# Kernel tuning notes

Measured on AMD Instinct MI355X. Metric: run time of the kernel, lower is better.

Reference implementation:

```python
import jax, jax.numpy as jnp
import numpy as np

D_MODEL = 1024
N_HEADS = 16
D_K = D_MODEL // N_HEADS


def setup_inputs() -> dict:
    key = jax.random.key(0)
    ks = jax.random.split(key, 10)
    B, L = 2, 2048
    s = 1.0 / np.sqrt(D_MODEL)
    inp = {
        "x": jax.random.normal(ks[0], (B, L, D_MODEL), dtype=jnp.float32),
        "bond_influence": jax.random.uniform(ks[1], (B, L, L), dtype=jnp.float32),
        "Wq": jax.random.uniform(ks[2], (D_MODEL, D_MODEL), jnp.float32, -s, s),
        "bq": jax.random.uniform(ks[3], (D_MODEL,), jnp.float32, -s, s),
        "Wk": jax.random.uniform(ks[4], (D_MODEL, D_MODEL), jnp.float32, -s, s),
        "bk": jax.random.uniform(ks[5], (D_MODEL,), jnp.float32, -s, s),
        "Wv": jax.random.uniform(ks[6], (D_MODEL, D_MODEL), jnp.float32, -s, s),
        "bv": jax.random.uniform(ks[7], (D_MODEL,), jnp.float32, -s, s),
        "Wo": jax.random.uniform(ks[8], (D_MODEL, D_MODEL), jnp.float32, -s, s),
        "bo": jax.random.uniform(ks[9], (D_MODEL,), jnp.float32, -s, s),
    }
    return inp


def reference(x, bond_influence, Wq, bq, Wk, bk, Wv, bv, Wo, bo):
    B, L, _ = x.shape
    # QKV projections -> [B, H, L, d_k]
    def proj(W, b):
        return (x @ W + b).reshape(B, L, N_HEADS, D_K).transpose(0, 2, 1, 3)
    Q = proj(Wq, bq)
    K = proj(Wk, bk)
    V = proj(Wv, bv)
    # scores: [B, H, L, L], scaled then modulated by per-batch bond influence
    scores = jnp.einsum('bhqd,bhkd->bhqk', Q, K) / jnp.sqrt(jnp.float32(D_K))
    scores = scores * bond_influence[:, None, :, :]
    attn = jax.nn.softmax(scores, axis=-1)
    out = jnp.einsum('bhqk,bhkd->bhqd', attn, V)  # [B, H, L, d_k]
    out = out.transpose(0, 2, 1, 3).reshape(B, L, D_MODEL)
    return out @ Wo + bo
```

## Files before the change

### kernel.cpp

```cpp
#include <hip/hip_runtime.h>
#include <stdint.h>

typedef unsigned short u16;
typedef __attribute__((ext_vector_type(8))) short bf16x8;
typedef __attribute__((ext_vector_type(4))) float f32x4;

__device__ __forceinline__ u16 f2bf(float f) {
    union { float f; uint32_t u; } v; v.f = f;
    uint32_t u = v.u + 0x7fffu + ((v.u >> 16) & 1u);
    return (u16)(u >> 16);
}
__device__ __forceinline__ float vexp2(float x) {
    float d;
    asm("v_exp_f32 %0, %1" : "=v"(d) : "v"(x));
    return d;
}
__device__ __forceinline__ uint32_t cvtpk(float a, float b) {
    uint32_t d;
    asm("v_cvt_pk_bf16_f32 %0, %1, %2" : "=v"(d) : "v"(a), "v"(b));
    return d;
}

__device__ __forceinline__ void gld16(const void* g, void* l) {
    __builtin_amdgcn_global_load_lds((const __attribute__((address_space(1))) void*)g,
                                     (__attribute__((address_space(3))) void*)l,
                                     16, 0, 0);
}

__device__ __forceinline__ void plswap16(uint32_t& a, uint32_t& b) {
    asm volatile("v_permlane16_swap_b32 %0, %1" : "+v"(a), "+v"(b));
}


__global__ void cvt_bf16_kernel(const float* __restrict__ s, u16* __restrict__ d, int n4,
                                float scale) {
    int i = blockIdx.x * blockDim.x + threadIdx.x;
    const int stride = gridDim.x * blockDim.x;
    for (; i < n4; i += stride) {
        float4 v = ((const float4*)s)[i];
        ushort4 o;
        o.x = f2bf(v.x * scale); o.y = f2bf(v.y * scale);
        o.z = f2bf(v.z * scale); o.w = f2bf(v.w * scale);
        ((ushort4*)d)[i] = o;
    }
}

__global__ void transpose4_bf16_kernel(const float* __restrict__ Wq, const float* __restrict__ Wk,
                                       const float* __restrict__ Wv, const float* __restrict__ Wo,
                                       u16* __restrict__ dqkv, u16* __restrict__ dо) {
    __shared__ float tile[32][33];
    const int z = blockIdx.z;
    const float* src = (z == 0) ? Wq : (z == 1) ? Wk : (z == 2) ? Wv : Wo;
    u16* dst = (z < 3) ? (dqkv + (size_t)z * 1024 * 1024) : dо;
    const int tx = threadIdx.x, ty = threadIdx.y;
    const int bx = blockIdx.x * 32, by = blockIdx.y * 32;
#pragma unroll
    for (int i = ty; i < 32; i += 8)
        tile[i][tx] = src[(size_t)(by + i) * 1024 + bx + tx];
    __syncthreads();
#pragma unroll
    for (int i = ty; i < 32; i += 8)
        dst[(size_t)(bx + i) * 1024 + by + tx] = f2bf(tile[tx][i]);
}


template <int EPI>
__global__ __launch_bounds__(256) void gemm128(
    const u16* __restrict__ A, const u16* __restrict__ Bt,
    const float* __restrict__ bias0, const float* __restrict__ bias1,
    const float* __restrict__ bias2,
    u16* __restrict__ o_q, u16* __restrict__ o_k, u16* __restrict__ o_vt,
    float* __restrict__ o_f)
{
    constexpr int K = 1024;
    __shared__ u16 As[128 * 32];
    __shared__ u16 Bs[128 * 32];
    const int t = threadIdx.x;
    const int lane = t & 63, w = t >> 6;
    const int wm = w >> 1, wn = w & 1;
    const int g = lane >> 4, r = lane & 15;
    const int mbase = blockIdx.y * 128, nbase = blockIdx.x * 128;

    const f32x4 zero4 = {0.f, 0.f, 0.f, 0.f};
    f32x4 acc[4][4];
#pragma unroll
    for (int m = 0; m < 4; ++m)
#pragma unroll
        for (int n = 0; n < 4; ++n) acc[m][n] = zero4;

    for (int k0 = 0; k0 < K; k0 += 32) {
#pragma unroll
        for (int i = 0; i < 2; ++i) {
            const int base = i * 256 + (w << 6);
            const int idx = base + lane;
            const int row = idx >> 2, cc = (idx & 3) << 3;
            gld16(A + (size_t)(mbase + row) * K + k0 + cc, (char*)As + base * 16);
            gld16(Bt + (size_t)(nbase + row) * K + k0 + cc, (char*)Bs + base * 16);
        }
        __syncthreads();

        bf16x8 af[4], bfr[4];
#pragma unroll
        for (int m = 0; m < 4; ++m)
            af[m] = *(const bf16x8*)&As[(wm * 64 + m * 16 + r) * 32 + g * 8];
#pragma unroll
        for (int n = 0; n < 4; ++n)
            bfr[n] = *(const bf16x8*)&Bs[(wn * 64 + n * 16 + r) * 32 + g * 8];
        __builtin_amdgcn_s_setprio(1);
#pragma unroll
        for (int m = 0; m < 4; ++m)
#pragma unroll
            for (int n = 0; n < 4; ++n)
                acc[m][n] = __builtin_amdgcn_mfma_f32_16x16x32_bf16(af[m], bfr[n], acc[m][n], 0, 0, 0);
        __builtin_amdgcn_s_setprio(0);
        __syncthreads();
    }

#pragma unroll
    for (int m = 0; m < 4; ++m) {
#pragma unroll
        for (int n = 0; n < 4; ++n) {
            const int c = nbase + wn * 64 + n * 16 + r;
#pragma unroll
            for (int j = 0; j < 4; ++j) {
                const int rr = mbase + wm * 64 + m * 16 + g * 4 + j;
                const float y = acc[m][n][j];
                if (EPI == 0) {
                    const int which = c >> 10, d = c & 1023;
                    const int b = rr >> 11, l = rr & 2047;
                    const int h = d >> 6, dd = d & 63;
                    const size_t bh = (size_t)(b * 16 + h);
                    if (which == 0) {
                        o_q[(bh * 2048 + l) * 64 + dd] = f2bf((y + bias0[d]) * 0.18033688011112042f);
                    } else if (which == 1) {
                        o_k[(bh * 2048 + l) * 64 + dd] = f2bf(y + bias1[d]);
                    } else {
                        o_vt[(bh * 64 + dd) * 2048 + l] = f2bf(y + bias2[d]);
                    }
                } else {
                    o_f[(size_t)rr * 1024 + c] = y + bias0[c];
                }
            }
        }
    }
}


#define ATTN_STEP(CUR, BD, BDN, PREF, WAITN)                                                 \
    {                                                                                        \
        if (PREF) {                                                                          \
            const int kt2 = kt + 64;                                                         \
            _Pragma("unroll")                                                                \
            for (int i = 0; i < 4; ++i) {                                                    \
                const int idx = i * 128 + t;                                                 \
                const int row = idx >> 3, ch = idx & 7;                                      \
                const int chg = ch ^ (row & 7);                                              \
                gld16(kb + kvBase + (size_t)(kt2 + row) * 64 + chg * 8,                      \
                      (char*)&Ks[CUR ^ 1][0] + idx * 16);                                    \
                gld16(vtb + vtBase + (size_t)row * 2048 + kt2 + chg * 8,                     \
                      (char*)&Vs[CUR ^ 1][0] + idx * 16);                                    \
            }                                                                                \
            _Pragma("unroll")                                                                \
            for (int qf = 0; qf < 2; ++qf)                                                   \
                _Pragma("unroll")                                                            \
                for (int kf = 0; kf < 4; ++kf)                                               \
                    BDN[qf][kf] = *(const float4*)&bondf[bondRow0 + (size_t)qf * 32768 +     \
                                                         kt2 + kf * 16 + g * 4];             \
        }                                                                                    \
        asm volatile("s_waitcnt vmcnt(" #WAITN ")" ::: "memory");                            \
        __builtin_amdgcn_s_barrier();                                                        \
        __builtin_amdgcn_sched_barrier(0);                                                   \
                                                                            \
        f32x4 st[2][4];                                                                      \
        {                                                                                    \
            bf16x8 kfr[2][2];                                                                \
            _Pragma("unroll")                                                                \
            for (int kz = 0; kz < 2; ++kz)                                                   \
                _Pragma("unroll")                                                            \
                for (int kf = 0; kf < 2; ++kf)                                               \
                    kfr[kz][kf] = *(const bf16x8*)((const char*)&Ks[CUR][0] +                \
                                    (kf * 16 + r) * 128 + (((kz * 4 + g) ^ sw) * 16));       \
            _Pragma("unroll")                                                                \
            for (int qf = 0; qf < 2; ++qf)                                                   \
                _Pragma("unroll")                                                            \
                for (int kf = 0; kf < 2; ++kf) st[qf][kf] = zero4;                           \
            __builtin_amdgcn_s_setprio(1);                                                   \
            _Pragma("unroll")                                                                \
            for (int kz = 0; kz < 2; ++kz)                                                   \
                _Pragma("unroll")                                                            \
                for (int qf = 0; qf < 2; ++qf)                                               \
                    _Pragma("unroll")                                                        \
                    for (int kf = 0; kf < 2; ++kf)                                           \
                        st[qf][kf] = __builtin_amdgcn_mfma_f32_16x16x32_bf16(                \
                            kfr[kz][kf], aq[qf][kz], st[qf][kf], 0, 0, 0);                   \
            __builtin_amdgcn_s_setprio(0);                                                   \
        }                                                                                    \
                                                                      \
        bf16x8 ap0[2], ap1[2];                                                               \
        _Pragma("unroll")                                                                    \
        for (int qf = 0; qf < 2; ++qf) {                                                     \
            uint32_t pkl[2], pkh[2];                                                         \
            _Pragma("unroll")                                                                \
            for (int kf = 0; kf < 2; ++kf) {                                                 \
                const float p0 = vexp2(st[qf][kf][0] * BD[qf][kf].x);                        \
                const float p1 = vexp2(st[qf][kf][1] * BD[qf][kf].y);                        \
                const float p2 = vexp2(st[qf][kf][2] * BD[qf][kf].z);                        \
                const float p3 = vexp2(st[qf][kf][3] * BD[qf][kf].w);                        \
                sm[qf] += (p0 + p1) + (p2 + p3);                                             \
                pkl[kf] = cvtpk(p0, p1);                                                     \
                pkh[kf] = cvtpk(p2, p3);                                                     \
            }                                                                                \
            plswap16(pkl[0], pkl[1]);                                                        \
            plswap16(pkh[0], pkh[1]);                                                        \
            union { uint32_t u[4]; bf16x8 v; } a_;                                           \
            a_.u[0] = pkl[0]; a_.u[1] = pkh[0]; a_.u[2] = pkl[1]; a_.u[3] = pkh[1];          \
            ap0[qf] = a_.v;                                                                  \
        }                                                                                    \
                                                                            \
        {                                                                                    \
            bf16x8 kfr[2][2];                                                                \
            _Pragma("unroll")                                                                \
            for (int kz = 0; kz < 2; ++kz)                                                   \
                _Pragma("unroll")                                                            \
                for (int kf = 0; kf < 2; ++kf)                                               \
                    kfr[kz][kf] = *(const bf16x8*)((const char*)&Ks[CUR][0] +                \
                                    ((kf + 2) * 16 + r) * 128 + (((kz * 4 + g) ^ sw) * 16)); \
            _Pragma("unroll")                                                                \
            for (int qf = 0; qf < 2; ++qf)                                                   \
                _Pragma("unroll")                                                            \
                for (int kf = 0; kf < 2; ++kf) st[qf][kf + 2] = zero4;                       \
            __builtin_amdgcn_s_setprio(1);                                                   \
            _Pragma("unroll")                                                                \
            for (int kz = 0; kz < 2; ++kz)                                                   \
                _Pragma("unroll")                                                            \
                for (int qf = 0; qf < 2; ++qf)                                               \
                    _Pragma("unroll")                                                        \
                    for (int kf = 0; kf < 2; ++kf)                                           \
                        st[qf][kf + 2] = __builtin_amdgcn_mfma_f32_16x16x32_bf16(            \
                            kfr[kz][kf], aq[qf][kz], st[qf][kf + 2], 0, 0, 0);               \
            __builtin_amdgcn_s_setprio(0);                                                   \
        }                                                                                    \
                                                                                \
        {                                                                                    \
            bf16x8 bv_[4];                                                                   \
            _Pragma("unroll")                                                                \
            for (int nf = 0; nf < 4; ++nf)                                                   \
                bv_[nf] = *(const bf16x8*)((const char*)&Vs[CUR][0] +                        \
                            (nf * 16 + r) * 128 + ((pg ^ sw) * 16));                         \
            __builtin_amdgcn_s_setprio(1);                                                   \
            _Pragma("unroll")                                                                \
            for (int qf = 0; qf < 2; ++qf)                                                   \
                _Pragma("unroll")                                                            \
                for (int nf = 0; nf < 4; ++nf)                                               \
                    o[qf][nf] = __builtin_amdgcn_mfma_f32_16x16x32_bf16(                     \
                        ap0[qf], bv_[nf], o[qf][nf], 0, 0, 0);                               \
            __builtin_amdgcn_s_setprio(0);                                                   \
        }                                                                                    \
                                                                      \
        _Pragma("unroll")                                                                    \
        for (int qf = 0; qf < 2; ++qf) {                                                     \
            uint32_t pkl[2], pkh[2];                                                         \
            _Pragma("unroll")                                                                \
            for (int kf = 0; kf < 2; ++kf) {                                                 \
                const float p0 = vexp2(st[qf][kf + 2][0] * BD[qf][kf + 2].x);                \
                const float p1 = vexp2(st[qf][kf + 2][1] * BD[qf][kf + 2].y);                \
                const float p2 = vexp2(st[qf][kf + 2][2] * BD[qf][kf + 2].z);                \
                const float p3 = vexp2(st[qf][kf + 2][3] * BD[qf][kf + 2].w);                \
                sm[qf] += (p0 + p1) + (p2 + p3);                                             \
                pkl[kf] = cvtpk(p0, p1);                                                     \
                pkh[kf] = cvtpk(p2, p3);                                                     \
            }                                                                                \
            plswap16(pkl[0], pkl[1]);                                                        \
            plswap16(pkh[0], pkh[1]);                                                        \
            union { uint32_t u[4]; bf16x8 v; } a_;                                           \
            a_.u[0] = pkl[0]; a_.u[1] = pkh[0]; a_.u[2] = pkl[1]; a_.u[3] = pkh[1];          \
            ap1[qf] = a_.v;                                                                  \
        }                                                                                    \
                                                                                \
        {                                                                                    \
            bf16x8 bv_[4];                                                                   \
            _Pragma("unroll")                                                                \
            for (int nf = 0; nf < 4; ++nf)                                                   \
                bv_[nf] = *(const bf16x8*)((const char*)&Vs[CUR][0] +                        \
                            (nf * 16 + r) * 128 + (((4 + pg) ^ sw) * 16));                   \
            __builtin_amdgcn_s_setprio(1);                                                   \
            _Pragma("unroll")                                                                \
            for (int qf = 0; qf < 2; ++qf)                                                   \
                _Pragma("unroll")                                                            \
                for (int nf = 0; nf < 4; ++nf)                                               \
                    o[qf][nf] = __builtin_amdgcn_mfma_f32_16x16x32_bf16(                     \
                        ap1[qf], bv_[nf], o[qf][nf], 0, 0, 0);                               \
            __builtin_amdgcn_s_setprio(0);                                                   \
        }                                                                                    \
        __builtin_amdgcn_sched_barrier(0);                                                   \
        __builtin_amdgcn_s_barrier();                                                        \
        kt += 64;                                                                            \
    }

__global__ __launch_bounds__(128, 2) void attn_kernel(
    const u16* __restrict__ qb, const u16* __restrict__ kb,
    const u16* __restrict__ vtb, const float* __restrict__ bondf,
    u16* __restrict__ attnout)
{
    __shared__ u16 Ks[2][64 * 64];
    __shared__ u16 Vs[2][64 * 64];
    const int t = threadIdx.x;
    const int lane = t & 63, w = t >> 6;
    const int g = lane >> 4, r = lane & 15;
    const int sw = r & 7;
    const int pg = ((g & 1) << 1) | (g >> 1);
    const int flat = blockIdx.x;
    const int x = flat & 7;
    const int j = flat >> 3;
    const int b = x >> 2;
    const int qt = (x & 3) * 8 + (j & 7);
    const int h = j >> 3;
    const int bh = b * 16 + h;
    const int q0 = qt * 64 + w * 32;
    const size_t kvBase = (size_t)bh * 2048 * 64;
    const size_t vtBase = (size_t)bh * 64 * 2048;
    const size_t bondRow0 = ((size_t)b * 2048 + q0 + r) * 2048;

    bf16x8 aq[2][2];
#pragma unroll
    for (int qf = 0; qf < 2; ++qf)
#pragma unroll
        for (int kz = 0; kz < 2; ++kz)
            aq[qf][kz] = *(const bf16x8*)&qb[kvBase + (size_t)(q0 + qf * 16 + r) * 64 + kz * 32 + g * 8];

    const f32x4 zero4 = {0.f, 0.f, 0.f, 0.f};
    f32x4 o[2][4];
#pragma unroll
    for (int qf = 0; qf < 2; ++qf)
#pragma unroll
        for (int nf = 0; nf < 4; ++nf) o[qf][nf] = zero4;
    float sm[2] = {0.f, 0.f};

#pragma unroll
    for (int i = 0; i < 4; ++i) {
        const int idx = i * 128 + t;
        const int row = idx >> 3, ch = idx & 7;
        const int chg = ch ^ (row & 7);
        gld16(kb + kvBase + (size_t)row * 64 + chg * 8, (char*)&Ks[0][0] + idx * 16);
        gld16(vtb + vtBase + (size_t)row * 2048 + chg * 8, (char*)&Vs[0][0] + idx * 16);
    }
    float4 bdA[2][4], bdB[2][4];
#pragma unroll
    for (int qf = 0; qf < 2; ++qf)
#pragma unroll
        for (int kf = 0; kf < 4; ++kf)
            bdA[qf][kf] = *(const float4*)&bondf[bondRow0 + (size_t)qf * 32768 + kf * 16 + g * 4];

    int kt = 0;
    for (int s = 0; s < 15; ++s) {
        ATTN_STEP(0, bdA, bdB, 1, 16)
        ATTN_STEP(1, bdB, bdA, 1, 16)
    }
    ATTN_STEP(0, bdA, bdB, 1, 16)
    ATTN_STEP(1, bdB, bdA, 0, 0)

#pragma unroll
    for (int qf = 0; qf < 2; ++qf) {
        sm[qf] += __shfl_xor(sm[qf], 16, 64);
        sm[qf] += __shfl_xor(sm[qf], 32, 64);
    }
#pragma unroll
    for (int qf = 0; qf < 2; ++qf)
#pragma unroll
        for (int j2 = 0; j2 < 4; ++j2) {
            const float inv = 1.f / __shfl(sm[qf], g * 4 + j2, 16);
            const size_t orow = ((size_t)b * 2048 + q0 + qf * 16 + g * 4 + j2) * 1024 + h * 64;
#pragma unroll
            for (int nf = 0; nf < 4; ++nf)
                attnout[orow + nf * 16 + r] = f2bf(o[qf][nf][j2] * inv);
        }
}


extern "C" void kernel_launch(void* const* d_in, const int* in_sizes, int n_in,
                              void* d_out, int out_size, void* d_ws, size_t ws_size,
                              hipStream_t stream) {
    (void)in_sizes; (void)n_in; (void)out_size; (void)ws_size;
    const float* x    = (const float*)d_in[0];
    const float* bond = (const float*)d_in[1];
    const float* Wq   = (const float*)d_in[2];
    const float* bq   = (const float*)d_in[3];
    const float* Wk   = (const float*)d_in[4];
    const float* bk   = (const float*)d_in[5];
    const float* Wv   = (const float*)d_in[6];
    const float* bv   = (const float*)d_in[7];
    const float* Wo   = (const float*)d_in[8];
    const float* bo   = (const float*)d_in[9];
    float* out = (float*)d_out;

    char* ws = (char*)d_ws;
    u16* xb      = (u16*)(ws);
    u16* wqkvt   = (u16*)(ws + 8388608);
    u16* wot     = (u16*)(ws + 14680064);
    u16* qb      = (u16*)(ws + 16777216);
    u16* kb_     = (u16*)(ws + 25165824);
    u16* vtb     = (u16*)(ws + 33554432);
    u16* attnout = (u16*)(ws + 58720256);

    dim3 tb(32, 8);
    transpose4_bf16_kernel<<<dim3(32, 32, 4), tb, 0, stream>>>(Wq, Wk, Wv, Wo, wqkvt, wot);
    cvt_bf16_kernel<<<1024, 256, 0, stream>>>(x, xb, 4194304 / 4, 1.0f);

    gemm128<0><<<dim3(24, 32), 256, 0, stream>>>(xb, wqkvt, bq, bk, bv, qb, kb_, vtb, nullptr);
    attn_kernel<<<dim3(1024), 128, 0, stream>>>(qb, kb_, vtb, bond, attnout);
    gemm128<1><<<dim3(8, 32), 256, 0, stream>>>(attnout, wot, bo, nullptr, nullptr,
                                                nullptr, nullptr, nullptr, out);
}
```

Measured before the change: 163.1 us.

## Deepen GEMM K-tile to 64 with swizzled LDS, XCD-aware block mapping, fuse pack kernels

The GEMM K-step grows from 32 to 64 so there are half as many barrier pairs per tile. LDS chunks are XOR-swizzled to avoid bank conflicts on the wider rows. A 1D grid is remapped so consecutive blocks land on the same XCD and share A/B tiles in L2. The weight-transpose and x-conversion kernels are merged into one launch. LDS use doubles per block, which may reduce occupancy.

```diff
diff --git a/kernel.cpp b/kernel.cpp
--- a/kernel.cpp
+++ b/kernel.cpp
@@ -32,27 +32,29 @@
 }
 
 
-__global__ void cvt_bf16_kernel(const float* __restrict__ s, u16* __restrict__ d, int n4,
-                                float scale) {
-    int i = blockIdx.x * blockDim.x + threadIdx.x;
-    const int stride = gridDim.x * blockDim.x;
-    for (; i < n4; i += stride) {
-        float4 v = ((const float4*)s)[i];
-        ushort4 o;
-        o.x = f2bf(v.x * scale); o.y = f2bf(v.y * scale);
-        o.z = f2bf(v.z * scale); o.w = f2bf(v.w * scale);
-        ((ushort4*)d)[i] = o;
-    }
-}
-
-__global__ void transpose4_bf16_kernel(const float* __restrict__ Wq, const float* __restrict__ Wk,
-                                       const float* __restrict__ Wv, const float* __restrict__ Wo,
-                                       u16* __restrict__ dqkv, u16* __restrict__ dо) {
+__global__ void pack5_kernel(const float* __restrict__ Wq, const float* __restrict__ Wk,
+                             const float* __restrict__ Wv, const float* __restrict__ Wo,
+                             const float* __restrict__ x,
+                             u16* __restrict__ dqkv, u16* __restrict__ dwo,
+                             u16* __restrict__ dx) {
+    const int z = blockIdx.z;
+    const int tx = threadIdx.x, ty = threadIdx.y;
+    if (z == 4) {
+        const int bid = blockIdx.y * 32 + blockIdx.x;
+        const int tid = ty * 32 + tx;
+#pragma unroll
+        for (int i = 0; i < 4; ++i) {
+            const int idx = bid * 1024 + i * 256 + tid;
+            float4 v = ((const float4*)x)[idx];
+            ushort4 o;
+            o.x = f2bf(v.x); o.y = f2bf(v.y); o.z = f2bf(v.z); o.w = f2bf(v.w);
+            ((ushort4*)dx)[idx] = o;
+        }
+        return;
+    }
     __shared__ float tile[32][33];
-    const int z = blockIdx.z;
     const float* src = (z == 0) ? Wq : (z == 1) ? Wk : (z == 2) ? Wv : Wo;
-    u16* dst = (z < 3) ? (dqkv + (size_t)z * 1024 * 1024) : dо;
-    const int tx = threadIdx.x, ty = threadIdx.y;
+    u16* dst = (z < 3) ? (dqkv + (size_t)z * 1024 * 1024) : dwo;
     const int bx = blockIdx.x * 32, by = blockIdx.y * 32;
 #pragma unroll
     for (int i = ty; i < 32; i += 8)
@@ -70,16 +72,20 @@
     const float* __restrict__ bias0, const float* __restrict__ bias1,
     const float* __restrict__ bias2,
     u16* __restrict__ o_q, u16* __restrict__ o_k, u16* __restrict__ o_vt,
-    float* __restrict__ o_f)
+    float* __restrict__ o_f, int nbx)
 {
     constexpr int K = 1024;
-    __shared__ u16 As[128 * 32];
-    __shared__ u16 Bs[128 * 32];
+    __shared__ u16 As[128 * 64];
+    __shared__ u16 Bs[128 * 64];
     const int t = threadIdx.x;
     const int lane = t & 63, w = t >> 6;
     const int wm = w >> 1, wn = w & 1;
     const int g = lane >> 4, r = lane & 15;
-    const int mbase = blockIdx.y * 128, nbase = blockIdx.x * 128;
+    const int sw = r & 7;
+    const int f = blockIdx.x;
+    const int cpx = (gridDim.x >> 3);
+    const int swz = (f & 7) * cpx + (f >> 3);
+    const int mbase = (swz / nbx) * 128, nbase = (swz % nbx) * 128;
 
     const f32x4 zero4 = {0.f, 0.f, 0.f, 0.f};
     f32x4 acc[4][4];
@@ -88,31 +94,38 @@
 #pragma unroll
         for (int n = 0; n < 4; ++n) acc[m][n] = zero4;
 
-    for (int k0 = 0; k0 < K; k0 += 32) {
-#pragma unroll
-        for (int i = 0; i < 2; ++i) {
-            const int base = i * 256 + (w << 6);
-            const int idx = base + lane;
-            const int row = idx >> 2, cc = (idx & 3) << 3;
-            gld16(A + (size_t)(mbase + row) * K + k0 + cc, (char*)As + base * 16);
-            gld16(Bt + (size_t)(nbase + row) * K + k0 + cc, (char*)Bs + base * 16);
+    for (int k0 = 0; k0 < K; k0 += 64) {
+#pragma unroll
+        for (int i = 0; i < 4; ++i) {
+            const int idx = i * 256 + t;
+            const int row = idx >> 3, ch = idx & 7;
+            const int chg = ch ^ (row & 7);
+            gld16(A + (size_t)(mbase + row) * K + k0 + chg * 8, (char*)As + idx * 16);
+            gld16(Bt + (size_t)(nbase + row) * K + k0 + chg * 8, (char*)Bs + idx * 16);
         }
         __syncthreads();
 
-        bf16x8 af[4], bfr[4];
-#pragma unroll
-        for (int m = 0; m < 4; ++m)
-            af[m] = *(const bf16x8*)&As[(wm * 64 + m * 16 + r) * 32 + g * 8];
-#pragma unroll
-        for (int n = 0; n < 4; ++n)
-            bfr[n] = *(const bf16x8*)&Bs[(wn * 64 + n * 16 + r) * 32 + g * 8];
-        __builtin_amdgcn_s_setprio(1);
-#pragma unroll
-        for (int m = 0; m < 4; ++m)
-#pragma unroll
-            for (int n = 0; n < 4; ++n)
-                acc[m][n] = __builtin_amdgcn_mfma_f32_16x16x32_bf16(af[m], bfr[n], acc[m][n], 0, 0, 0);
-        __builtin_amdgcn_s_setprio(0);
+#pragma unroll
+        for (int kk = 0; kk < 2; ++kk) {
+            bf16x8 af[4], bfr[4];
+#pragma unroll
+            for (int m = 0; m < 4; ++m) {
+                const int row = wm * 64 + m * 16 + r;
+                af[m] = *(const bf16x8*)((const char*)As + row * 128 + (((kk * 4 + g) ^ sw) << 4));
+            }
+#pragma unroll
+            for (int n = 0; n < 4; ++n) {
+                const int row = wn * 64 + n * 16 + r;
+                bfr[n] = *(const bf16x8*)((const char*)Bs + row * 128 + (((kk * 4 + g) ^ sw) << 4));
+            }
+            __builtin_amdgcn_s_setprio(1);
+#pragma unroll
+            for (int m = 0; m < 4; ++m)
+#pragma unroll
+                for (int n = 0; n < 4; ++n)
+                    acc[m][n] = __builtin_amdgcn_mfma_f32_16x16x32_bf16(af[m], bfr[n], acc[m][n], 0, 0, 0);
+            __builtin_amdgcn_s_setprio(0);
+        }
         __syncthreads();
     }
 
@@ -402,12 +415,10 @@
     u16* vtb     = (u16*)(ws + 33554432);
     u16* attnout = (u16*)(ws + 58720256);
 
-    dim3 tb(32, 8);
-    transpose4_bf16_kernel<<<dim3(32, 32, 4), tb, 0, stream>>>(Wq, Wk, Wv, Wo, wqkvt, wot);
-    cvt_bf16_kernel<<<1024, 256, 0, stream>>>(x, xb, 4194304 / 4, 1.0f);
-
-    gemm128<0><<<dim3(24, 32), 256, 0, stream>>>(xb, wqkvt, bq, bk, bv, qb, kb_, vtb, nullptr);
+    pack5_kernel<<<dim3(32, 32, 5), dim3(32, 8), 0, stream>>>(Wq, Wk, Wv, Wo, x, wqkvt, wot, xb);
+
+    gemm128<0><<<dim3(768), 256, 0, stream>>>(xb, wqkvt, bq, bk, bv, qb, kb_, vtb, nullptr, 24);
     attn_kernel<<<dim3(1024), 128, 0, stream>>>(qb, kb_, vtb, bond, attnout);
-    gemm128<1><<<dim3(8, 32), 256, 0, stream>>>(attnout, wot, bo, nullptr, nullptr,
-                                                nullptr, nullptr, nullptr, out);
-}
+    gemm128<1><<<dim3(256), 256, 0, stream>>>(attnout, wot, bo, nullptr, nullptr,
+                                              nullptr, nullptr, nullptr, out, 8);
+}
```

Result: faster. 153.5 us, median of 3 (-5.9%).
